# Kernel tuning notes

Hardware: AMD Instinct MI355X
Metric: run time of the kernel (lower is better)

Reference implementation:

```python
import jax, jax.numpy as jnp
import numpy as np

INPUT_SIZE = 512
HIDDEN = 1024
NUM_CLASSES = 1000
BATCH = 64
SEQ = 512


def setup_inputs() -> dict:
    key = jax.random.key(0)
    ks = jax.random.split(key, 12)
    comb = INPUT_SIZE + HIDDEN
    s = 1.0 / np.sqrt(comb)
    sf = 1.0 / np.sqrt(HIDDEN)
    return {
        "x": jax.random.normal(ks[0], (BATCH, SEQ, INPUT_SIZE), dtype=jnp.float32),
        "Wz_w": jax.random.uniform(ks[1], (HIDDEN, comb), jnp.float32, -s, s),
        "Wz_b": jax.random.uniform(ks[2], (HIDDEN,), jnp.float32, -s, s),
        "Wr_w": jax.random.uniform(ks[3], (HIDDEN, comb), jnp.float32, -s, s),
        "Wr_b": jax.random.uniform(ks[4], (HIDDEN,), jnp.float32, -s, s),
        "Wc_w": jax.random.uniform(ks[5], (HIDDEN, comb), jnp.float32, -s, s),
        "Wc_b": jax.random.uniform(ks[6], (HIDDEN,), jnp.float32, -s, s),
        "Wo_w": jax.random.uniform(ks[7], (HIDDEN, comb), jnp.float32, -s, s),
        "Wo_b": jax.random.uniform(ks[8], (HIDDEN,), jnp.float32, -s, s),
        "fc_w": jax.random.uniform(ks[9], (NUM_CLASSES, HIDDEN), jnp.float32, -sf, sf),
        "fc_b": jax.random.uniform(ks[10], (NUM_CLASSES,), jnp.float32, -sf, sf),
    }


def reference(x, Wz_w, Wz_b, Wr_w, Wr_b, Wc_w, Wc_b, Wo_w, Wo_b, fc_w, fc_b):
    B, T, _ = x.shape
    H = Wz_w.shape[0]

    def step(carry, x_t):
        h, c = carry
        combined = jnp.concatenate([x_t, h], axis=1)          # [B, I+H]
        z = jax.nn.sigmoid(combined @ Wz_w.T + Wz_b)
        r = jax.nn.sigmoid(combined @ Wr_w.T + Wr_b)
        combined_reset = jnp.concatenate([x_t, r * c], axis=1)
        c_tilde = jnp.tanh(combined_reset @ Wc_w.T + Wc_b)
        c_new = z * c + (1.0 - z) * c_tilde
        o = jax.nn.sigmoid(combined @ Wo_w.T + Wo_b)
        h_new = o * jnp.tanh(c_new)
        return (h_new, c_new), None

    h0 = jnp.zeros((B, H), dtype=x.dtype)
    c0 = jnp.zeros((B, H), dtype=x.dtype)
    xs = jnp.swapaxes(x, 0, 1)                                # [T, B, I]
    (h, c), _ = jax.lax.scan(step, (h0, c0), xs)
    # dropout is identity (p=0 / eval mode)
    return h @ fc_w.T + fc_b                                  # [B, num_classes]
```

## Files before the change

kernel.cpp:

```cpp
#include <hip/hip_runtime.h>

#define NWG 128
#define TSTEPS 512

typedef __attribute__((ext_vector_type(8))) short short8;
typedef __attribute__((ext_vector_type(4))) float f32x4;

#define T0_OFF   0
#define T1_OFF   49152
#define T2_OFF   98304
#define RED_OFF  131072
#define ZBUF_OFF 135168
#define OBUF_OFF 137216
#define XCB_OFF  139264
#define CST_OFF  141312
#define RCS_OFF  143360
#define HST_OFF  145408
#define BIAS_OFF 147456
#define LDS_BYTES 147584

__device__ inline unsigned short f2bf(float f) {
  unsigned int b = __float_as_uint(f);
  return (unsigned short)((b + 0x7FFFu + ((b >> 16) & 1u)) >> 16);
}
__device__ inline float sigm(float x) { return 1.f / (1.f + __expf(-x)); }
__device__ inline float tanh_f(float x) { float e = __expf(2.f * x); return 1.f - 2.f / (e + 1.f); }

__device__ inline void cstore16(void* p, short8 v) {
  asm volatile("global_store_dwordx4 %0, %1, off sc0 sc1" :: "v"(p), "v"(v) : "memory");
}
__device__ inline void cstore4(void* p, int v) {
  asm volatile("global_store_dword %0, %1, off sc0 sc1" :: "v"(p), "v"(v) : "memory");
}
__device__ inline int cload4(const void* p) {
  int v;
  asm volatile("global_load_dword %0, %1, off sc0 sc1\n\ts_waitcnt vmcnt(0)"
               : "=&v"(v) : "v"(p) : "memory");
  return v;
}
__device__ inline void vmdrain() {
  asm volatile("s_waitcnt vmcnt(0)" ::: "memory");
}

__device__ inline void cload24(const unsigned short* p0, const unsigned short* p1, short8* a) {
  asm volatile(
    "global_load_dwordx4 %0,  %24, off sc0 sc1\n\t"
    "global_load_dwordx4 %1,  %24, off offset:64 sc0 sc1\n\t"
    "global_load_dwordx4 %2,  %24, off offset:128 sc0 sc1\n\t"
    "global_load_dwordx4 %3,  %24, off offset:192 sc0 sc1\n\t"
    "global_load_dwordx4 %4,  %24, off offset:256 sc0 sc1\n\t"
    "global_load_dwordx4 %5,  %24, off offset:320 sc0 sc1\n\t"
    "global_load_dwordx4 %6,  %24, off offset:384 sc0 sc1\n\t"
    "global_load_dwordx4 %7,  %24, off offset:448 sc0 sc1\n\t"
    "global_load_dwordx4 %8,  %24, off offset:512 sc0 sc1\n\t"
    "global_load_dwordx4 %9,  %24, off offset:576 sc0 sc1\n\t"
    "global_load_dwordx4 %10, %24, off offset:640 sc0 sc1\n\t"
    "global_load_dwordx4 %11, %24, off offset:704 sc0 sc1\n\t"
    "global_load_dwordx4 %12, %24, off offset:768 sc0 sc1\n\t"
    "global_load_dwordx4 %13, %24, off offset:832 sc0 sc1\n\t"
    "global_load_dwordx4 %14, %24, off offset:896 sc0 sc1\n\t"
    "global_load_dwordx4 %15, %24, off offset:960 sc0 sc1\n\t"
    "global_load_dwordx4 %16, %25, off sc0 sc1\n\t"
    "global_load_dwordx4 %17, %25, off offset:64 sc0 sc1\n\t"
    "global_load_dwordx4 %18, %25, off offset:128 sc0 sc1\n\t"
    "global_load_dwordx4 %19, %25, off offset:192 sc0 sc1\n\t"
    "global_load_dwordx4 %20, %25, off offset:256 sc0 sc1\n\t"
    "global_load_dwordx4 %21, %25, off offset:320 sc0 sc1\n\t"
    "global_load_dwordx4 %22, %25, off offset:384 sc0 sc1\n\t"
    "global_load_dwordx4 %23, %25, off offset:448 sc0 sc1\n\t"
    "s_waitcnt vmcnt(0)"
    : "=&v"(a[0]), "=&v"(a[1]), "=&v"(a[2]), "=&v"(a[3]),
      "=&v"(a[4]), "=&v"(a[5]), "=&v"(a[6]), "=&v"(a[7]),
      "=&v"(a[8]), "=&v"(a[9]), "=&v"(a[10]), "=&v"(a[11]),
      "=&v"(a[12]), "=&v"(a[13]), "=&v"(a[14]), "=&v"(a[15]),
      "=&v"(a[16]), "=&v"(a[17]), "=&v"(a[18]), "=&v"(a[19]),
      "=&v"(a[20]), "=&v"(a[21]), "=&v"(a[22]), "=&v"(a[23])
    : "v"(p0), "v"(p1)
    : "memory");
}

__device__ inline void cload16(const unsigned short* p, short8* a) {
  asm volatile(
    "global_load_dwordx4 %0,  %16, off sc0 sc1\n\t"
    "global_load_dwordx4 %1,  %16, off offset:64 sc0 sc1\n\t"
    "global_load_dwordx4 %2,  %16, off offset:128 sc0 sc1\n\t"
    "global_load_dwordx4 %3,  %16, off offset:192 sc0 sc1\n\t"
    "global_load_dwordx4 %4,  %16, off offset:256 sc0 sc1\n\t"
    "global_load_dwordx4 %5,  %16, off offset:320 sc0 sc1\n\t"
    "global_load_dwordx4 %6,  %16, off offset:384 sc0 sc1\n\t"
    "global_load_dwordx4 %7,  %16, off offset:448 sc0 sc1\n\t"
    "global_load_dwordx4 %8,  %16, off offset:512 sc0 sc1\n\t"
    "global_load_dwordx4 %9,  %16, off offset:576 sc0 sc1\n\t"
    "global_load_dwordx4 %10, %16, off offset:640 sc0 sc1\n\t"
    "global_load_dwordx4 %11, %16, off offset:704 sc0 sc1\n\t"
    "global_load_dwordx4 %12, %16, off offset:768 sc0 sc1\n\t"
    "global_load_dwordx4 %13, %16, off offset:832 sc0 sc1\n\t"
    "global_load_dwordx4 %14, %16, off offset:896 sc0 sc1\n\t"
    "global_load_dwordx4 %15, %16, off offset:960 sc0 sc1\n\t"
    "s_waitcnt vmcnt(0)"
    : "=&v"(a[0]), "=&v"(a[1]), "=&v"(a[2]), "=&v"(a[3]),
      "=&v"(a[4]), "=&v"(a[5]), "=&v"(a[6]), "=&v"(a[7]),
      "=&v"(a[8]), "=&v"(a[9]), "=&v"(a[10]), "=&v"(a[11]),
      "=&v"(a[12]), "=&v"(a[13]), "=&v"(a[14]), "=&v"(a[15])
    : "v"(p)
    : "memory");
}

__global__ void __launch_bounds__(256) lmgru_kernel(
    const float* __restrict__ x,
    const float* __restrict__ Wz, const float* __restrict__ bz,
    const float* __restrict__ Wr, const float* __restrict__ br,
    const float* __restrict__ Wc, const float* __restrict__ bc,
    const float* __restrict__ Wo, const float* __restrict__ bo,
    const float* __restrict__ fcw, const float* __restrict__ fcb,
    float* __restrict__ out, char* __restrict__ ws)
{
  extern __shared__ char lds[];
  const int tid  = threadIdx.x;
  const int wg   = blockIdx.x;
  const int lane = tid & 63;
  const int q    = tid >> 6;

  unsigned short* hbuf  = (unsigned short*)ws;
  unsigned short* rcbuf = (unsigned short*)(ws + 262144);
  unsigned short* xring = (unsigned short*)(ws + 524288);
  float*          h32   = (float*)(ws + 655360);
  int* hflagA  = (int*)(ws + 917504);
  int* hflagB  = hflagA + 128;
  int* rcflagA = hflagA + 256;
  int* rcflagB = hflagA + 384;
  int* hflag[2]  = {hflagA, hflagB};
  int* rcflag[2] = {rcflagA, rcflagB};

  float* zbuf = (float*)(lds + ZBUF_OFF);
  float* obuf = (float*)(lds + OBUF_OFF);
  float* xcb  = (float*)(lds + XCB_OFF);
  float* cst  = (float*)(lds + CST_OFF);
  float* rcs  = (float*)(lds + RCS_OFF);
  float* hst  = (float*)(lds + HST_OFF);
  float* bias = (float*)(lds + BIAS_OFF);

  const float* Wg[4] = {Wz, Wr, Wo, Wc};

  for (int it = 0; it < 12; ++it) {
    int slot = tid + 256 * it;
    int s = slot >> 6, l = slot & 63;
    int nn = l & 15, kg = (l >> 4) & 3;
    int k = 32 * s + kg * 8;
    int g = (nn < 8) ? 0 : 1;
    const float* src = Wg[g] + (8 * wg + (nn & 7)) * 1536 + k;
    short8 pk;
    #pragma unroll
    for (int j = 0; j < 8; ++j) pk[j] = (short)f2bf(src[j]);
    *(short8*)(lds + T0_OFF + s * 1024 + l * 16) = pk;
  }
  for (int it = 0; it < 12; ++it) {
    int slot = tid + 256 * it;
    int s = slot >> 6, l = slot & 63;
    int nn = l & 15, kg = (l >> 4) & 3;
    int k = 32 * s + kg * 8;
    int g = (nn < 8) ? 2 : 3;
    short8 pk = {};
    if (g == 2 || k < 512) {
      const float* src = Wg[g] + (8 * wg + (nn & 7)) * 1536 + k;
      #pragma unroll
      for (int j = 0; j < 8; ++j) pk[j] = (short)f2bf(src[j]);
    }
    *(short8*)(lds + T1_OFF + s * 1024 + l * 16) = pk;
  }
  for (int it = 0; it < 8; ++it) {
    int slot = tid + 256 * it;
    int s = slot >> 6, l = slot & 63;
    int nn = l & 15, kg = (l >> 4) & 3;
    int k = 32 * s + kg * 8;
    short8 pk = {};
    if (nn < 8) {
      const float* src = Wc + (8 * wg + nn) * 1536 + 512 + k;
      #pragma unroll
      for (int j = 0; j < 8; ++j) pk[j] = (short)f2bf(src[j]);
    }
    *(short8*)(lds + T2_OFF + s * 1024 + l * 16) = pk;
  }
  if (tid < 32) {
    const float* Bg[4] = {bz, br, bo, bc};
    bias[tid] = Bg[tid >> 3][8 * wg + (tid & 7)];
  }
  cst[tid] = 0.f; cst[tid + 256] = 0.f;
  if (tid < 64) {
    short8 z8 = {};
    cstore16(hbuf + tid * 1024 + 8 * wg, z8);
  }
  if (tid < 32) {
    int e = wg * 256 + tid * 8;
    int b = e >> 9, f = e & 511;
    const float* xs = x + b * 262144 + f;
    short8 pk;
    #pragma unroll
    for (int j = 0; j < 8; ++j) pk[j] = (short)f2bf(xs[j]);
    cstore16(xring + 32768 + b * 512 + f, pk);
  }
  __syncthreads();
  if (tid == 0) {
    vmdrain();
    cstore4(&hflagA[wg], 0);
    cstore4(&hflagB[wg], 0);
    cstore4(&rcflagA[wg], 0);
    cstore4(&rcflagB[wg], 0);
  }

  const int m   = q & 1;
  const int kh  = q >> 1;
  const int nn  = lane & 15;
  const int kg8 = ((lane >> 4) & 3) * 8;
  const int rbase = ((lane >> 4) & 3) * 4;

  for (int t = 1; t <= TSTEPS; ++t) {
    const int pc = t & 1, pp = (t - 1) & 1;

    for (int X = 0; X < 2; ++X) {
      if (tid < 128) {
        const int* fp = &hflag[X][tid];
        while (cload4(fp) < t - 1) __builtin_amdgcn_s_sleep(1);
      }
      __syncthreads();

      const int bbase = 32 * X;
      const int brow  = bbase + 16 * m + nn;
      f32x4 acc0 = {0.f, 0.f, 0.f, 0.f}, acc1 = {0.f, 0.f, 0.f, 0.f};
      const unsigned short* xr = xring + pc * 32768 + brow * 512;
      const unsigned short* hb = hbuf + pp * 65536 + brow * 1024;
      const unsigned short* p0 = kh ? (hb + 256 + kg8) : (xr + kg8);
      const unsigned short* p1 = kh ? (hb + 768 + kg8) : (hb + kg8);
      short8 af[24];
      cload24(p0, p1, af);
      #pragma unroll
      for (int j = 0; j < 24; ++j) {
        int s = 24 * kh + j;
        short8 b0 = *(const short8*)(lds + T0_OFF + s * 1024 + lane * 16);
        short8 b1 = *(const short8*)(lds + T1_OFF + s * 1024 + lane * 16);
        acc0 = __builtin_amdgcn_mfma_f32_16x16x32_bf16(af[j], b0, acc0, 0, 0, 0);
        acc1 = __builtin_amdgcn_mfma_f32_16x16x32_bf16(af[j], b1, acc1, 0, 0, 0);
      }
      if (kh == 1) {
        *(f32x4*)(lds + RED_OFF + ((m * 2 + 0) * 64 + lane) * 16) = acc0;
        *(f32x4*)(lds + RED_OFF + ((m * 2 + 1) * 64 + lane) * 16) = acc1;
      }
      __syncthreads();
      if (kh == 0) {
        acc0 += *(const f32x4*)(lds + RED_OFF + ((m * 2 + 0) * 64 + lane) * 16);
        acc1 += *(const f32x4*)(lds + RED_OFF + ((m * 2 + 1) * 64 + lane) * 16);
        #pragma unroll
        for (int i = 0; i < 4; ++i) {
          int b = bbase + 16 * m + rbase + i;
          float v0 = acc0[i] + bias[nn];
          float v1 = acc1[i] + bias[16 + nn];
          if (nn < 8) {
            zbuf[nn * 64 + b] = sigm(v0);
            obuf[nn * 64 + b] = sigm(v1);
          } else {
            int u = nn - 8;
            rcs[u * 64 + b] = sigm(v0) * cst[u * 64 + b];
            xcb[u * 64 + b] = v1;
          }
        }
      }
      __syncthreads();
      if (tid < 32) {
        int b = bbase + tid;
        short8 pk;
        #pragma unroll
        for (int u = 0; u < 8; ++u) pk[u] = (short)f2bf(rcs[u * 64 + b]);
        cstore16(rcbuf + pc * 65536 + b * 1024 + 8 * wg, pk);
      }
      if (tid == 0) {
        vmdrain();
        cstore4(&rcflag[X][wg], t);
      }
    }

    for (int X = 0; X < 2; ++X) {
      if (tid < 128) {
        const int* fp = &rcflag[X][tid];
        while (cload4(fp) < t) __builtin_amdgcn_s_sleep(1);
      }
      __syncthreads();

      const int bbase = 32 * X;
      const int brow  = bbase + 16 * m + nn;
      f32x4 acc = {0.f, 0.f, 0.f, 0.f};
      const unsigned short* rb = rcbuf + pc * 65536 + brow * 1024;
      short8 af[16];
      cload16(rb + kg8 + (kh ? 512 : 0), af);
      #pragma unroll
      for (int j = 0; j < 16; ++j) {
        int s = 16 * kh + j;
        short8 bf = *(const short8*)(lds + T2_OFF + s * 1024 + lane * 16);
        acc = __builtin_amdgcn_mfma_f32_16x16x32_bf16(af[j], bf, acc, 0, 0, 0);
      }
      if (kh == 1) *(f32x4*)(lds + RED_OFF + (m * 64 + lane) * 16) = acc;
      __syncthreads();
      if (kh == 0 && nn < 8) {
        acc += *(const f32x4*)(lds + RED_OFF + (m * 64 + lane) * 16);
        #pragma unroll
        for (int i = 0; i < 4; ++i) {
          int b = bbase + 16 * m + rbase + i;
          float ct = tanh_f(acc[i] + xcb[nn * 64 + b]);
          float z  = zbuf[nn * 64 + b];
          float cn = z * cst[nn * 64 + b] + (1.f - z) * ct;
          cst[nn * 64 + b] = cn;
          hst[nn * 64 + b] = obuf[nn * 64 + b] * tanh_f(cn);
        }
      }
      __syncthreads();
      if (tid < 32) {
        int b = bbase + tid;
        if (t < TSTEPS) {
          short8 pk;
          #pragma unroll
          for (int u = 0; u < 8; ++u) pk[u] = (short)f2bf(hst[u * 64 + b]);
          cstore16(hbuf + pc * 65536 + b * 1024 + 8 * wg, pk);
        } else {
          #pragma unroll
          for (int u = 0; u < 8; ++u) h32[b * 1024 + 8 * wg + u] = hst[u * 64 + b];
        }
      }
      if (X == 0 && t < TSTEPS && tid < 32) {
        int e = wg * 256 + tid * 8;
        int b = e >> 9, f = e & 511;
        const float* xs = x + b * 262144 + t * 512 + f;
        short8 pk;
        #pragma unroll
        for (int j = 0; j < 8; ++j) pk[j] = (short)f2bf(xs[j]);
        cstore16(xring + ((t + 1) & 1) * 32768 + b * 512 + f, pk);
      }
      if (tid == 0) {
        if (t < TSTEPS) {
          vmdrain();
          cstore4(&hflag[X][wg], t);
        } else {
          __hip_atomic_store(&hflag[X][wg], t, __ATOMIC_RELEASE, __HIP_MEMORY_SCOPE_AGENT);
        }
      }
    }
  }

  if (tid < 128) {
    while (__hip_atomic_load(&hflagA[tid], __ATOMIC_RELAXED, __HIP_MEMORY_SCOPE_AGENT) < TSTEPS)
      __builtin_amdgcn_s_sleep(1);
    while (__hip_atomic_load(&hflagB[tid], __ATOMIC_RELAXED, __HIP_MEMORY_SCOPE_AGENT) < TSTEPS)
      __builtin_amdgcn_s_sleep(1);
  }
  __syncthreads();
  __builtin_amdgcn_fence(__ATOMIC_ACQUIRE, "agent");

  if (wg < 125) {
    for (int cc = 0; cc < 2; ++cc) {
      int c = 8 * wg + 2 * q + cc;
      const float* wrow = fcw + c * 1024;
      for (int b = 0; b < 64; ++b) {
        const float* hrow = h32 + b * 1024;
        float s = 0.f;
        for (int kk = lane; kk < 1024; kk += 64) s = __builtin_fmaf(hrow[kk], wrow[kk], s);
        #pragma unroll
        for (int off = 32; off; off >>= 1) s += __shfl_xor(s, off);
        if (lane == 0) out[b * 1000 + c] = s + fcb[c];
      }
    }
  }
}

extern "C" void kernel_launch(void* const* d_in, const int* in_sizes, int n_in,
                              void* d_out, int out_size, void* d_ws, size_t ws_size,
                              hipStream_t stream) {
  (void)in_sizes; (void)n_in; (void)out_size; (void)ws_size;
  const float* x   = (const float*)d_in[0];
  const float* Wz  = (const float*)d_in[1];
  const float* bz  = (const float*)d_in[2];
  const float* Wr  = (const float*)d_in[3];
  const float* br  = (const float*)d_in[4];
  const float* Wc  = (const float*)d_in[5];
  const float* bc  = (const float*)d_in[6];
  const float* Wo  = (const float*)d_in[7];
  const float* bo  = (const float*)d_in[8];
  const float* fcw = (const float*)d_in[9];
  const float* fcb = (const float*)d_in[10];

  hipFuncSetAttribute((const void*)lmgru_kernel,
                      hipFuncAttributeMaxDynamicSharedMemorySize, LDS_BYTES);

  hipLaunchKernelGGL(lmgru_kernel, dim3(NWG), dim3(256), LDS_BYTES, stream,
                     x, Wz, bz, Wr, br, Wc, bc, Wo, bo, fcw, fcb,
                     (float*)d_out, (char*)d_ws);
}
```

Before: 9.916 ms.

## Replace per-WG flag arrays with global atomic counters and drop K-split reduction

Swaps the per-workgroup flag polling, where 128 threads each spin on a flag, for two global atomic counters that a single thread polls against 128*t. Each timestep now handles all 64 batch rows in one pass instead of two 32-row halves. Each wave now covers the full K range for 16 rows, so the LDS partial-sum reduction and its extra barriers are gone. The cost is fewer parallel waves per MFMA chain, more registers held per wave, and atomic contention on a single counter from 128 WGs.

```diff
diff --git a/kernel.cpp b/kernel.cpp
--- a/kernel.cpp
+++ b/kernel.cpp
@@ -9,7 +9,6 @@
 #define T0_OFF   0
 #define T1_OFF   49152
 #define T2_OFF   98304
-#define RED_OFF  131072
 #define ZBUF_OFF 135168
 #define OBUF_OFF 137216
 #define XCB_OFF  139264
@@ -29,6 +28,9 @@
 __device__ inline void cstore16(void* p, short8 v) {
   asm volatile("global_store_dwordx4 %0, %1, off sc0 sc1" :: "v"(p), "v"(v) : "memory");
 }
+__device__ inline void cstore16f(void* p, f32x4 v) {
+  asm volatile("global_store_dwordx4 %0, %1, off sc0 sc1" :: "v"(p), "v"(v) : "memory");
+}
 __device__ inline void cstore4(void* p, int v) {
   asm volatile("global_store_dword %0, %1, off sc0 sc1" :: "v"(p), "v"(v) : "memory");
 }
@@ -42,44 +44,100 @@
   asm volatile("s_waitcnt vmcnt(0)" ::: "memory");
 }
 
-__device__ inline void cload24(const unsigned short* p0, const unsigned short* p1, short8* a) {
+__device__ inline void cload32_nw(const unsigned short* p, short8* a) {
   asm volatile(
-    "global_load_dwordx4 %0,  %24, off sc0 sc1\n\t"
-    "global_load_dwordx4 %1,  %24, off offset:64 sc0 sc1\n\t"
-    "global_load_dwordx4 %2,  %24, off offset:128 sc0 sc1\n\t"
-    "global_load_dwordx4 %3,  %24, off offset:192 sc0 sc1\n\t"
-    "global_load_dwordx4 %4,  %24, off offset:256 sc0 sc1\n\t"
-    "global_load_dwordx4 %5,  %24, off offset:320 sc0 sc1\n\t"
-    "global_load_dwordx4 %6,  %24, off offset:384 sc0 sc1\n\t"
-    "global_load_dwordx4 %7,  %24, off offset:448 sc0 sc1\n\t"
-    "global_load_dwordx4 %8,  %24, off offset:512 sc0 sc1\n\t"
-    "global_load_dwordx4 %9,  %24, off offset:576 sc0 sc1\n\t"
-    "global_load_dwordx4 %10, %24, off offset:640 sc0 sc1\n\t"
-    "global_load_dwordx4 %11, %24, off offset:704 sc0 sc1\n\t"
-    "global_load_dwordx4 %12, %24, off offset:768 sc0 sc1\n\t"
-    "global_load_dwordx4 %13, %24, off offset:832 sc0 sc1\n\t"
-    "global_load_dwordx4 %14, %24, off offset:896 sc0 sc1\n\t"
-    "global_load_dwordx4 %15, %24, off offset:960 sc0 sc1\n\t"
-    "global_load_dwordx4 %16, %25, off sc0 sc1\n\t"
-    "global_load_dwordx4 %17, %25, off offset:64 sc0 sc1\n\t"
-    "global_load_dwordx4 %18, %25, off offset:128 sc0 sc1\n\t"
-    "global_load_dwordx4 %19, %25, off offset:192 sc0 sc1\n\t"
-    "global_load_dwordx4 %20, %25, off offset:256 sc0 sc1\n\t"
-    "global_load_dwordx4 %21, %25, off offset:320 sc0 sc1\n\t"
-    "global_load_dwordx4 %22, %25, off offset:384 sc0 sc1\n\t"
-    "global_load_dwordx4 %23, %25, off offset:448 sc0 sc1\n\t"
+    "global_load_dwordx4 %0,  %32, off sc0 sc1\n\t"
+    "global_load_dwordx4 %1,  %32, off offset:64 sc0 sc1\n\t"
+    "global_load_dwordx4 %2,  %32, off offset:128 sc0 sc1\n\t"
+    "global_load_dwordx4 %3,  %32, off offset:192 sc0 sc1\n\t"
+    "global_load_dwordx4 %4,  %32, off offset:256 sc0 sc1\n\t"
+    "global_load_dwordx4 %5,  %32, off offset:320 sc0 sc1\n\t"
+    "global_load_dwordx4 %6,  %32, off offset:384 sc0 sc1\n\t"
+    "global_load_dwordx4 %7,  %32, off offset:448 sc0 sc1\n\t"
+    "global_load_dwordx4 %8,  %32, off offset:512 sc0 sc1\n\t"
+    "global_load_dwordx4 %9,  %32, off offset:576 sc0 sc1\n\t"
+    "global_load_dwordx4 %10, %32, off offset:640 sc0 sc1\n\t"
+    "global_load_dwordx4 %11, %32, off offset:704 sc0 sc1\n\t"
+    "global_load_dwordx4 %12, %32, off offset:768 sc0 sc1\n\t"
+    "global_load_dwordx4 %13, %32, off offset:832 sc0 sc1\n\t"
+    "global_load_dwordx4 %14, %32, off offset:896 sc0 sc1\n\t"
+    "global_load_dwordx4 %15, %32, off offset:960 sc0 sc1\n\t"
+    "global_load_dwordx4 %16, %32, off offset:1024 sc0 sc1\n\t"
+    "global_load_dwordx4 %17, %32, off offset:1088 sc0 sc1\n\t"
+    "global_load_dwordx4 %18, %32, off offset:1152 sc0 sc1\n\t"
+    "global_load_dwordx4 %19, %32, off offset:1216 sc0 sc1\n\t"
+    "global_load_dwordx4 %20, %32, off offset:1280 sc0 sc1\n\t"
+    "global_load_dwordx4 %21, %32, off offset:1344 sc0 sc1\n\t"
+    "global_load_dwordx4 %22, %32, off offset:1408 sc0 sc1\n\t"
+    "global_load_dwordx4 %23, %32, off offset:1472 sc0 sc1\n\t"
+    "global_load_dwordx4 %24, %32, off offset:1536 sc0 sc1\n\t"
+    "global_load_dwordx4 %25, %32, off offset:1600 sc0 sc1\n\t"
+    "global_load_dwordx4 %26, %32, off offset:1664 sc0 sc1\n\t"
+    "global_load_dwordx4 %27, %32, off offset:1728 sc0 sc1\n\t"
+    "global_load_dwordx4 %28, %32, off offset:1792 sc0 sc1\n\t"
+    "global_load_dwordx4 %29, %32, off offset:1856 sc0 sc1\n\t"
+    "global_load_dwordx4 %30, %32, off offset:1920 sc0 sc1\n\t"
+    "global_load_dwordx4 %31, %32, off offset:1984 sc0 sc1"
+    : "=&v"(a[0]), "=&v"(a[1]), "=&v"(a[2]), "=&v"(a[3]),
+      "=&v"(a[4]), "=&v"(a[5]), "=&v"(a[6]), "=&v"(a[7]),
+      "=&v"(a[8]), "=&v"(a[9]), "=&v"(a[10]), "=&v"(a[11]),
+      "=&v"(a[12]), "=&v"(a[13]), "=&v"(a[14]), "=&v"(a[15]),
+      "=&v"(a[16]), "=&v"(a[17]), "=&v"(a[18]), "=&v"(a[19]),
+      "=&v"(a[20]), "=&v"(a[21]), "=&v"(a[22]), "=&v"(a[23]),
+      "=&v"(a[24]), "=&v"(a[25]), "=&v"(a[26]), "=&v"(a[27]),
+      "=&v"(a[28]), "=&v"(a[29]), "=&v"(a[30]), "=&v"(a[31])
+    : "v"(p)
+    : "memory");
+}
+
+__device__ inline void cload32_w(const unsigned short* p, short8* a) {
+  asm volatile(
+    "global_load_dwordx4 %0,  %32, off sc0 sc1\n\t"
+    "global_load_dwordx4 %1,  %32, off offset:64 sc0 sc1\n\t"
+    "global_load_dwordx4 %2,  %32, off offset:128 sc0 sc1\n\t"
+    "global_load_dwordx4 %3,  %32, off offset:192 sc0 sc1\n\t"
+    "global_load_dwordx4 %4,  %32, off offset:256 sc0 sc1\n\t"
+    "global_load_dwordx4 %5,  %32, off offset:320 sc0 sc1\n\t"
+    "global_load_dwordx4 %6,  %32, off offset:384 sc0 sc1\n\t"
+    "global_load_dwordx4 %7,  %32, off offset:448 sc0 sc1\n\t"
+    "global_load_dwordx4 %8,  %32, off offset:512 sc0 sc1\n\t"
+    "global_load_dwordx4 %9,  %32, off offset:576 sc0 sc1\n\t"
+    "global_load_dwordx4 %10, %32, off offset:640 sc0 sc1\n\t"
+    "global_load_dwordx4 %11, %32, off offset:704 sc0 sc1\n\t"
+    "global_load_dwordx4 %12, %32, off offset:768 sc0 sc1\n\t"
+    "global_load_dwordx4 %13, %32, off offset:832 sc0 sc1\n\t"
+    "global_load_dwordx4 %14, %32, off offset:896 sc0 sc1\n\t"
+    "global_load_dwordx4 %15, %32, off offset:960 sc0 sc1\n\t"
+    "global_load_dwordx4 %16, %32, off offset:1024 sc0 sc1\n\t"
+    "global_load_dwordx4 %17, %32, off offset:1088 sc0 sc1\n\t"
+    "global_load_dwordx4 %18, %32, off offset:1152 sc0 sc1\n\t"
+    "global_load_dwordx4 %19, %32, off offset:1216 sc0 sc1\n\t"
+    "global_load_dwordx4 %20, %32, off offset:1280 sc0 sc1\n\t"
+    "global_load_dwordx4 %21, %32, off offset:1344 sc0 sc1\n\t"
+    "global_load_dwordx4 %22, %32, off offset:1408 sc0 sc1\n\t"
+    "global_load_dwordx4 %23, %32, off offset:1472 sc0 sc1\n\t"
+    "global_load_dwordx4 %24, %32, off offset:1536 sc0 sc1\n\t"
+    "global_load_dwordx4 %25, %32, off offset:1600 sc0 sc1\n\t"
+    "global_load_dwordx4 %26, %32, off offset:1664 sc0 sc1\n\t"
+    "global_load_dwordx4 %27, %32, off offset:1728 sc0 sc1\n\t"
+    "global_load_dwordx4 %28, %32, off offset:1792 sc0 sc1\n\t"
+    "global_load_dwordx4 %29, %32, off offset:1856 sc0 sc1\n\t"
+    "global_load_dwordx4 %30, %32, off offset:1920 sc0 sc1\n\t"
+    "global_load_dwordx4 %31, %32, off offset:1984 sc0 sc1\n\t"
     "s_waitcnt vmcnt(0)"
     : "=&v"(a[0]), "=&v"(a[1]), "=&v"(a[2]), "=&v"(a[3]),
       "=&v"(a[4]), "=&v"(a[5]), "=&v"(a[6]), "=&v"(a[7]),
       "=&v"(a[8]), "=&v"(a[9]), "=&v"(a[10]), "=&v"(a[11]),
       "=&v"(a[12]), "=&v"(a[13]), "=&v"(a[14]), "=&v"(a[15]),
       "=&v"(a[16]), "=&v"(a[17]), "=&v"(a[18]), "=&v"(a[19]),
-      "=&v"(a[20]), "=&v"(a[21]), "=&v"(a[22]), "=&v"(a[23])
-    : "v"(p0), "v"(p1)
+      "=&v"(a[20]), "=&v"(a[21]), "=&v"(a[22]), "=&v"(a[23]),
+      "=&v"(a[24]), "=&v"(a[25]), "=&v"(a[26]), "=&v"(a[27]),
+      "=&v"(a[28]), "=&v"(a[29]), "=&v"(a[30]), "=&v"(a[31])
+    : "v"(p)
     : "memory");
 }
 
-__device__ inline void cload16(const unsigned short* p, short8* a) {
+__device__ inline void cload16_w(const unsigned short* p, short8* a) {
   asm volatile(
     "global_load_dwordx4 %0,  %16, off sc0 sc1\n\t"
     "global_load_dwordx4 %1,  %16, off offset:64 sc0 sc1\n\t"
@@ -125,12 +183,9 @@
   unsigned short* rcbuf = (unsigned short*)(ws + 262144);
   unsigned short* xring = (unsigned short*)(ws + 524288);
   float*          h32   = (float*)(ws + 655360);
-  int* hflagA  = (int*)(ws + 917504);
-  int* hflagB  = hflagA + 128;
-  int* rcflagA = hflagA + 256;
-  int* rcflagB = hflagA + 384;
-  int* hflag[2]  = {hflagA, hflagB};
-  int* rcflag[2] = {rcflagA, rcflagB};
+  int* hctr     = (int*)(ws + 917504);
+  int* rcctr    = (int*)(ws + 917504 + 128);
+  int* initflag = (int*)(ws + 917504 + 256);
 
   float* zbuf = (float*)(lds + ZBUF_OFF);
   float* obuf = (float*)(lds + OBUF_OFF);
@@ -199,111 +254,103 @@
     for (int j = 0; j < 8; ++j) pk[j] = (short)f2bf(xs[j]);
     cstore16(xring + 32768 + b * 512 + f, pk);
   }
+  if (wg == 0 && tid == 0) {
+    cstore4(hctr, 0);
+    cstore4(rcctr, 0);
+  }
   __syncthreads();
   if (tid == 0) {
     vmdrain();
-    cstore4(&hflagA[wg], 0);
-    cstore4(&hflagB[wg], 0);
-    cstore4(&rcflagA[wg], 0);
-    cstore4(&rcflagB[wg], 0);
-  }
-
-  const int m   = q & 1;
-  const int kh  = q >> 1;
-  const int nn  = lane & 15;
-  const int kg8 = ((lane >> 4) & 3) * 8;
+    cstore4(&initflag[wg], 0);
+  }
+  if (tid < 128) {
+    const int* fp = &initflag[tid];
+    while (cload4(fp) < 0) __builtin_amdgcn_s_sleep(1);
+  }
+  __syncthreads();
+
+  const int nn    = lane & 15;
+  const int kg8   = ((lane >> 4) & 3) * 8;
   const int rbase = ((lane >> 4) & 3) * 4;
+  const int brow  = 16 * q + nn;
 
   for (int t = 1; t <= TSTEPS; ++t) {
     const int pc = t & 1, pp = (t - 1) & 1;
 
-    for (int X = 0; X < 2; ++X) {
-      if (tid < 128) {
-        const int* fp = &hflag[X][tid];
-        while (cload4(fp) < t - 1) __builtin_amdgcn_s_sleep(1);
-      }
-      __syncthreads();
-
-      const int bbase = 32 * X;
-      const int brow  = bbase + 16 * m + nn;
+    if (tid == 0) {
+      const int target = 128 * (t - 1);
+      while (cload4(hctr) < target) __builtin_amdgcn_s_sleep(1);
+    }
+    __syncthreads();
+
+    {
       f32x4 acc0 = {0.f, 0.f, 0.f, 0.f}, acc1 = {0.f, 0.f, 0.f, 0.f};
-      const unsigned short* xr = xring + pc * 32768 + brow * 512;
-      const unsigned short* hb = hbuf + pp * 65536 + brow * 1024;
-      const unsigned short* p0 = kh ? (hb + 256 + kg8) : (xr + kg8);
-      const unsigned short* p1 = kh ? (hb + 768 + kg8) : (hb + kg8);
-      short8 af[24];
-      cload24(p0, p1, af);
-      #pragma unroll
-      for (int j = 0; j < 24; ++j) {
-        int s = 24 * kh + j;
+      const unsigned short* hb = hbuf + pp * 65536 + brow * 1024 + kg8;
+      const unsigned short* xr = xring + pc * 32768 + brow * 512 + kg8;
+      short8 ah[32], ax[16];
+      cload32_nw(hb, ah);
+      cload16_w(xr, ax);
+      #pragma unroll
+      for (int s = 0; s < 16; ++s) {
         short8 b0 = *(const short8*)(lds + T0_OFF + s * 1024 + lane * 16);
         short8 b1 = *(const short8*)(lds + T1_OFF + s * 1024 + lane * 16);
-        acc0 = __builtin_amdgcn_mfma_f32_16x16x32_bf16(af[j], b0, acc0, 0, 0, 0);
-        acc1 = __builtin_amdgcn_mfma_f32_16x16x32_bf16(af[j], b1, acc1, 0, 0, 0);
-      }
-      if (kh == 1) {
-        *(f32x4*)(lds + RED_OFF + ((m * 2 + 0) * 64 + lane) * 16) = acc0;
-        *(f32x4*)(lds + RED_OFF + ((m * 2 + 1) * 64 + lane) * 16) = acc1;
-      }
-      __syncthreads();
-      if (kh == 0) {
-        acc0 += *(const f32x4*)(lds + RED_OFF + ((m * 2 + 0) * 64 + lane) * 16);
-        acc1 += *(const f32x4*)(lds + RED_OFF + ((m * 2 + 1) * 64 + lane) * 16);
+        acc0 = __builtin_amdgcn_mfma_f32_16x16x32_bf16(ax[s], b0, acc0, 0, 0, 0);
+        acc1 = __builtin_amdgcn_mfma_f32_16x16x32_bf16(ax[s], b1, acc1, 0, 0, 0);
+      }
+      #pragma unroll
+      for (int s = 16; s < 48; ++s) {
+        short8 b0 = *(const short8*)(lds + T0_OFF + s * 1024 + lane * 16);
+        short8 b1 = *(const short8*)(lds + T1_OFF + s * 1024 + lane * 16);
+        acc0 = __builtin_amdgcn_mfma_f32_16x16x32_bf16(ah[s - 16], b0, acc0, 0, 0, 0);
+        acc1 = __builtin_amdgcn_mfma_f32_16x16x32_bf16(ah[s - 16], b1, acc1, 0, 0, 0);
+      }
+      #pragma unroll
+      for (int i = 0; i < 4; ++i) {
+        int b = 16 * q + rbase + i;
+        float v0 = acc0[i] + bias[nn];
+        float v1 = acc1[i] + bias[16 + nn];
+        if (nn < 8) {
+          zbuf[nn * 64 + b] = sigm(v0);
+          obuf[nn * 64 + b] = sigm(v1);
+        } else {
+          int u = nn - 8;
+          rcs[u * 64 + b] = sigm(v0) * cst[u * 64 + b];
+          xcb[u * 64 + b] = v1;
+        }
+      }
+    }
+    __syncthreads();
+    if (tid < 64) {
+      short8 pk;
+      #pragma unroll
+      for (int u = 0; u < 8; ++u) pk[u] = (short)f2bf(rcs[u * 64 + tid]);
+      cstore16(rcbuf + pc * 65536 + tid * 1024 + 8 * wg, pk);
+    }
+    if (tid == 0) {
+      vmdrain();
+      __hip_atomic_fetch_add(rcctr, 1, __ATOMIC_RELAXED, __HIP_MEMORY_SCOPE_AGENT);
+    }
+
+    if (tid == 0) {
+      const int target = 128 * t;
+      while (cload4(rcctr) < target) __builtin_amdgcn_s_sleep(1);
+    }
+    __syncthreads();
+
+    {
+      f32x4 acc = {0.f, 0.f, 0.f, 0.f};
+      const unsigned short* rb = rcbuf + pc * 65536 + brow * 1024 + kg8;
+      short8 ar[32];
+      cload32_w(rb, ar);
+      #pragma unroll
+      for (int s = 0; s < 32; ++s) {
+        short8 bf = *(const short8*)(lds + T2_OFF + s * 1024 + lane * 16);
+        acc = __builtin_amdgcn_mfma_f32_16x16x32_bf16(ar[s], bf, acc, 0, 0, 0);
+      }
+      if (nn < 8) {
         #pragma unroll
         for (int i = 0; i < 4; ++i) {
-          int b = bbase + 16 * m + rbase + i;
-          float v0 = acc0[i] + bias[nn];
-          float v1 = acc1[i] + bias[16 + nn];
-          if (nn < 8) {
-            zbuf[nn * 64 + b] = sigm(v0);
-            obuf[nn * 64 + b] = sigm(v1);
-          } else {
-            int u = nn - 8;
-            rcs[u * 64 + b] = sigm(v0) * cst[u * 64 + b];
-            xcb[u * 64 + b] = v1;
-          }
-        }
-      }
-      __syncthreads();
-      if (tid < 32) {
-        int b = bbase + tid;
-        short8 pk;
-        #pragma unroll
-        for (int u = 0; u < 8; ++u) pk[u] = (short)f2bf(rcs[u * 64 + b]);
-        cstore16(rcbuf + pc * 65536 + b * 1024 + 8 * wg, pk);
-      }
-      if (tid == 0) {
-        vmdrain();
-        cstore4(&rcflag[X][wg], t);
-      }
-    }
-
-    for (int X = 0; X < 2; ++X) {
-      if (tid < 128) {
-        const int* fp = &rcflag[X][tid];
-        while (cload4(fp) < t) __builtin_amdgcn_s_sleep(1);
-      }
-      __syncthreads();
-
-      const int bbase = 32 * X;
-      const int brow  = bbase + 16 * m + nn;
-      f32x4 acc = {0.f, 0.f, 0.f, 0.f};
-      const unsigned short* rb = rcbuf + pc * 65536 + brow * 1024;
-      short8 af[16];
-      cload16(rb + kg8 + (kh ? 512 : 0), af);
-      #pragma unroll
-      for (int j = 0; j < 16; ++j) {
-        int s = 16 * kh + j;
-        short8 bf = *(const short8*)(lds + T2_OFF + s * 1024 + lane * 16);
-        acc = __builtin_amdgcn_mfma_f32_16x16x32_bf16(af[j], bf, acc, 0, 0, 0);
-      }
-      if (kh == 1) *(f32x4*)(lds + RED_OFF + (m * 64 + lane) * 16) = acc;
-      __syncthreads();
-      if (kh == 0 && nn < 8) {
-        acc += *(const f32x4*)(lds + RED_OFF + (m * 64 + lane) * 16);
-        #pragma unroll
-        for (int i = 0; i < 4; ++i) {
-          int b = bbase + 16 * m + rbase + i;
+          int b = 16 * q + rbase + i;
           float ct = tanh_f(acc[i] + xcb[nn * 64 + b]);
           float z  = zbuf[nn * 64 + b];
           float cn = z * cst[nn * 64 + b] + (1.f - z) * ct;
@@ -311,44 +358,39 @@
           hst[nn * 64 + b] = obuf[nn * 64 + b] * tanh_f(cn);
         }
       }
-      __syncthreads();
-      if (tid < 32) {
-        int b = bbase + tid;
-        if (t < TSTEPS) {
-          short8 pk;
-          #pragma unroll
-          for (int u = 0; u < 8; ++u) pk[u] = (short)f2bf(hst[u * 64 + b]);
-          cstore16(hbuf + pc * 65536 + b * 1024 + 8 * wg, pk);
-        } else {
-          #pragma unroll
-          for (int u = 0; u < 8; ++u) h32[b * 1024 + 8 * wg + u] = hst[u * 64 + b];
-        }
-      }
-      if (X == 0 && t < TSTEPS && tid < 32) {
-        int e = wg * 256 + tid * 8;
-        int b = e >> 9, f = e & 511;
-        const float* xs = x + b * 262144 + t * 512 + f;
+    }
+    __syncthreads();
+    if (t < TSTEPS && tid < 32) {
+      int e = wg * 256 + tid * 8;
+      int b = e >> 9, f = e & 511;
+      const float* xs = x + b * 262144 + t * 512 + f;
+      short8 pk;
+      #pragma unroll
+      for (int j = 0; j < 8; ++j) pk[j] = (short)f2bf(xs[j]);
+      cstore16(xring + ((t + 1) & 1) * 32768 + b * 512 + f, pk);
+    }
+    if (tid < 64) {
+      if (t < TSTEPS) {
         short8 pk;
         #pragma unroll
-        for (int j = 0; j < 8; ++j) pk[j] = (short)f2bf(xs[j]);
-        cstore16(xring + ((t + 1) & 1) * 32768 + b * 512 + f, pk);
-      }
-      if (tid == 0) {
-        if (t < TSTEPS) {
-          vmdrain();
-          cstore4(&hflag[X][wg], t);
-        } else {
-          __hip_atomic_store(&hflag[X][wg], t, __ATOMIC_RELEASE, __HIP_MEMORY_SCOPE_AGENT);
-        }
-      }
-    }
-  }
-
-  if (tid < 128) {
-    while (__hip_atomic_load(&hflagA[tid], __ATOMIC_RELAXED, __HIP_MEMORY_SCOPE_AGENT) < TSTEPS)
-      __builtin_amdgcn_s_sleep(1);
-    while (__hip_atomic_load(&hflagB[tid], __ATOMIC_RELAXED, __HIP_MEMORY_SCOPE_AGENT) < TSTEPS)
-      __builtin_amdgcn_s_sleep(1);
+        for (int u = 0; u < 8; ++u) pk[u] = (short)f2bf(hst[u * 64 + tid]);
+        cstore16(hbuf + pc * 65536 + tid * 1024 + 8 * wg, pk);
+      } else {
+        f32x4 lo, hi;
+        #pragma unroll
+        for (int u = 0; u < 4; ++u) { lo[u] = hst[u * 64 + tid]; hi[u] = hst[(u + 4) * 64 + tid]; }
+        cstore16f(h32 + tid * 1024 + 8 * wg, lo);
+        cstore16f(h32 + tid * 1024 + 8 * wg + 4, hi);
+      }
+    }
+    if (tid == 0) {
+      vmdrain();
+      __hip_atomic_fetch_add(hctr, 1, __ATOMIC_RELAXED, __HIP_MEMORY_SCOPE_AGENT);
+    }
+  }
+
+  if (tid == 0) {
+    while (cload4(hctr) < 128 * TSTEPS) __builtin_amdgcn_s_sleep(1);
   }
   __syncthreads();
   __builtin_amdgcn_fence(__ATOMIC_ACQUIRE, "agent");
```

Measured after the change: 10.81 ms. 1.09x slower.
